# Kernel tuning notes

Hardware: AMD Instinct MI355X
Metric: run time of the kernel (lower is better)

Reference implementation:

```python
import jax, jax.numpy as jnp
import numpy as np

EPS = 1e-6

def gram_schmidt_orthonormalize(U, eps=EPS):
    # U: [B, K, D] -> orthonormalized along K, vectorized over batch
    B, K, D = U.shape
    vs = []
    for i in range(K):
        v = U[:, i]  # [B, D]
        for vj in vs:
            coeff = jnp.sum(v * vj, axis=1, keepdims=True) / (jnp.sum(vj * vj, axis=1, keepdims=True) + eps)
            v = v - coeff * vj
        norm = jnp.maximum(jnp.linalg.norm(v, axis=1, keepdims=True), eps)
        vs.append(v / norm)
    return jnp.stack(vs, axis=1)  # [B, K, D]

def setup_inputs() -> dict:
    key = jax.random.key(0)
    ks = jax.random.split(key, 14)
    B, IN, H1, H2, OUT, E, G = 4096, 1024, 2048, 2048, 512, 8, 256
    s = 0.02
    return {
        "x":   jax.random.normal(ks[0], (B, IN), jnp.float32),
        "W1":  jax.random.normal(ks[1], (E, IN, H1), jnp.float32) * s,
        "b1":  jnp.zeros((E, H1), jnp.float32),
        "W2":  jax.random.normal(ks[2], (E, H1, H2), jnp.float32) * s,
        "b2":  jnp.zeros((E, H2), jnp.float32),
        "W3":  jax.random.normal(ks[3], (E, H2, OUT), jnp.float32) * s,
        "b3":  jnp.zeros((E, OUT), jnp.float32),
        "Wg1": jax.random.normal(ks[4], (IN, G), jnp.float32) * s,
        "bg1": jnp.zeros((G,), jnp.float32),
        "Wg2": jax.random.normal(ks[5], (G, E), jnp.float32) * s,
        "bg2": jnp.zeros((E,), jnp.float32),
        "Wo":  jax.random.normal(ks[6], (OUT, 1), jnp.float32) * s,
        "bo":  jnp.zeros((1,), jnp.float32),
    }

def reference(x, W1, b1, W2, b2, W3, b3, Wg1, bg1, Wg2, bg2, Wo, bo):
    # Expert MLPs, batched over expert axis e: [B,E,h]
    h = jax.nn.relu(jnp.einsum('bi,eih->beh', x, W1) + b1)
    h = jax.nn.relu(jnp.einsum('beh,ehk->bek', h, W2) + b2)
    expert_outputs = jnp.einsum('bek,ekd->bed', h, W3) + b3  # [B, E, D]
    # Gating network: MLP + softmax over experts
    g = jax.nn.relu(x @ Wg1 + bg1)
    gate_weights = jax.nn.softmax(g @ Wg2 + bg2, axis=-1)  # [B, E]
    # Per-sample Gram-Schmidt across experts, weighted combine
    ortho = gram_schmidt_orthonormalize(expert_outputs)  # [B, E, D]
    combined = jnp.einsum('bed,be->bd', ortho, gate_weights)  # [B, D]
    final = combined @ Wo + bo  # [B, 1]
    return (final, 0.0)
```

## Files before the change

### kernel.cpp

```cpp
#include <hip/hip_runtime.h>
#include <hip/hip_bf16.h>

#define DEVINL __device__ __forceinline__

constexpr int Bsz = 4096, INF = 1024, H1 = 2048, H2 = 2048, OUTD = 512, NE = 8, G = 256;

typedef __attribute__((ext_vector_type(8))) short bf16x8;
typedef __attribute__((ext_vector_type(4))) float f32x4;
typedef __attribute__((ext_vector_type(16))) float f32x16;
typedef unsigned short u16;

DEVINL u16 f2bf(float f) {
  unsigned int u = __float_as_uint(f);
  u = (u + 0x7FFFu + ((u >> 16) & 1u)) >> 16;
  return (u16)u;
}
DEVINL float bf2f(u16 h) { return __uint_as_float((unsigned int)h << 16); }

DEVINL void gload16(const void* g, void* l) {
  __builtin_amdgcn_global_load_lds(
      (const __attribute__((address_space(1))) void*)g,
      (__attribute__((address_space(3))) void*)l, 16, 0, 0);
}

DEVINL float waveAllSum(float v) {
#pragma unroll
  for (int m = 32; m > 0; m >>= 1) v += __shfl_xor(v, m, 64);
  return v;
}

DEVINL f32x16 mfma3(bf16x8 bh, bf16x8 bl, bf16x8 ah, bf16x8 al, f32x16 c) {
  c = __builtin_amdgcn_mfma_f32_32x32x16_bf16(bh, ah, c, 0, 0, 0);
  c = __builtin_amdgcn_mfma_f32_32x32x16_bf16(bl, ah, c, 0, 0, 0);
  c = __builtin_amdgcn_mfma_f32_32x32x16_bf16(bh, al, c, 0, 0, 0);
  return c;
}

__global__ __launch_bounds__(256) void pack_wt(const float* __restrict__ W,
                                               u16* __restrict__ Th,
                                               u16* __restrict__ Tl,
                                               int K, int N) {
  __shared__ float t[32][33];
  const int e = blockIdx.z;
  W += (size_t)e * K * N;
  Th += (size_t)e * N * K;
  Tl += (size_t)e * N * K;
  const int n0 = blockIdx.x * 32, k0 = blockIdx.y * 32;
  const int r = threadIdx.x >> 3, c = (threadIdx.x & 7) * 4;
  float4 v = *(const float4*)&W[(size_t)(k0 + r) * N + n0 + c];
  t[r][c + 0] = v.x; t[r][c + 1] = v.y; t[r][c + 2] = v.z; t[r][c + 3] = v.w;
  __syncthreads();
  float o0 = t[c + 0][r], o1 = t[c + 1][r], o2 = t[c + 2][r], o3 = t[c + 3][r];
  short4 h, l;
  h.x = f2bf(o0); l.x = f2bf(o0 - bf2f(h.x));
  h.y = f2bf(o1); l.y = f2bf(o1 - bf2f(h.y));
  h.z = f2bf(o2); l.z = f2bf(o2 - bf2f(h.z));
  h.w = f2bf(o3); l.w = f2bf(o3 - bf2f(h.w));
  *(short4*)&Th[(size_t)(n0 + r) * K + k0 + c] = h;
  *(short4*)&Tl[(size_t)(n0 + r) * K + k0 + c] = l;
}

__global__ __launch_bounds__(512, 2) void gemm_2bar(
    const u16* __restrict__ Ahi, const u16* __restrict__ Alo,
    const u16* __restrict__ Bhi, const u16* __restrict__ Blo,
    const float* __restrict__ bias,
    u16* __restrict__ Chi, u16* __restrict__ Clo,
    int M, int N, int K, size_t strideAe) {
  const int e = blockIdx.x;
  Ahi += (size_t)e * strideAe;
  Alo += (size_t)e * strideAe;
  Bhi += (size_t)e * (size_t)N * K;
  Blo += (size_t)e * (size_t)N * K;
  bias += (size_t)e * N;
  Chi += (size_t)e * (size_t)M * N;
  Clo += (size_t)e * (size_t)M * N;

  const int bm = blockIdx.y * 256, bn = blockIdx.z * 256;
  __shared__ __align__(16) char ldsb[163840];
  const int lane = threadIdx.x & 63, wid = threadIdx.x >> 6;
  const int wm = wid >> 2, wn = wid & 3;
  const int l15 = lane & 15, l4 = lane >> 4;
  const int bhalf = wn >> 1, jn = wn & 1;

  f32x4 acc[8][4];
#pragma unroll
  for (int i = 0; i < 8; ++i)
#pragma unroll
    for (int j = 0; j < 4; ++j) acc[i][j] = (f32x4){0.f, 0.f, 0.f, 0.f};

  const int nt = K / 32;

  auto stageA = [&](const u16* src, int T, int slot, int ldsOp) {
#pragma unroll
    for (int q = 0; q < 2; ++q) {
      const int g = wid * 2 + q;
      gload16(src + (size_t)(bm + g * 16 + l15) * K + T * 32 + l4 * 8,
              ldsb + ldsOp + slot * 16384 + g * 1024);
    }
  };
  auto stageB = [&](int T, int h) {
    const int s = T & 1;
#pragma unroll
    for (int q = 0; q < 2; ++q) {
      const int g = wid * 2 + q;
      const u16* src = (g < 8) ? Bhi : Blo;
      const int f = g & 7;
      gload16(src + (size_t)(bn + h * 128 + f * 16 + l15) * K + T * 32 + l4 * 8,
              ldsb + ((g < 8) ? 98304 : 131072) + s * 16384 + h * 8192 + f * 1024);
    }
  };

  bf16x8 ah[4], al[4], bh[4], bl[4];
  auto readA = [&](int slot, int ih) {
#pragma unroll
    for (int i = 0; i < 4; ++i) {
      const int off = slot * 16384 + wm * 8192 + (ih * 4 + i) * 1024 + lane * 16;
      ah[i] = *(const bf16x8*)(ldsb + off);
      al[i] = *(const bf16x8*)(ldsb + 49152 + off);
    }
  };
  auto readBall = [&](int sB) {
#pragma unroll
    for (int j = 0; j < 4; ++j) {
      const int off = sB * 16384 + bhalf * 8192 + (jn * 4 + j) * 1024 + lane * 16;
      bh[j] = *(const bf16x8*)(ldsb + 98304 + off);
      bl[j] = *(const bf16x8*)(ldsb + 131072 + off);
    }
  };

#define QUAD48(IH)                                                             \
  _Pragma("unroll") for (int i = 0; i < 4; ++i) {                              \
    _Pragma("unroll") for (int j = 0; j < 4; ++j) {                            \
      f32x4 a = acc[(IH)*4 + i][j];                                            \
      a = __builtin_amdgcn_mfma_f32_16x16x32_bf16(bh[j], ah[i], a, 0, 0, 0);   \
      a = __builtin_amdgcn_mfma_f32_16x16x32_bf16(bl[j], ah[i], a, 0, 0, 0);   \
      a = __builtin_amdgcn_mfma_f32_16x16x32_bf16(bh[j], al[i], a, 0, 0, 0);   \
      acc[(IH)*4 + i][j] = a;                                                  \
    }                                                                          \
  }

  stageB(0, 0); stageB(0, 1);
  stageA(Ahi, 0, 0, 0); stageA(Alo, 0, 0, 49152);
  stageB(1, 0); stageB(1, 1);
  stageA(Ahi, 1, 1, 0); stageA(Alo, 1, 1, 49152);
  asm volatile("s_waitcnt vmcnt(8)" ::: "memory");
  __builtin_amdgcn_sched_barrier(0);
  __builtin_amdgcn_s_barrier();
  __builtin_amdgcn_sched_barrier(0);

  int aS = 0, aS2 = 2;
  for (int t = 0; t < nt - 2; ++t) {
    const int sB = t & 1;
    readA(aS, 0);
    readBall(sB);
    __builtin_amdgcn_sched_barrier(0);
    stageA(Ahi, t + 2, aS2, 0); stageA(Alo, t + 2, aS2, 49152);
    QUAD48(0);
    __builtin_amdgcn_sched_barrier(0);
    __builtin_amdgcn_s_barrier();
    __builtin_amdgcn_sched_barrier(0);
    readA(aS, 1);
    __builtin_amdgcn_sched_barrier(0);
    stageB(t + 2, 0); stageB(t + 2, 1);
    QUAD48(1);
    asm volatile("s_waitcnt vmcnt(8)" ::: "memory");
    __builtin_amdgcn_sched_barrier(0);
    __builtin_amdgcn_s_barrier();
    __builtin_amdgcn_sched_barrier(0);
    aS = (aS == 2) ? 0 : aS + 1;
    aS2 = (aS2 == 2) ? 0 : aS2 + 1;
  }
  {
    const int sB = (nt - 2) & 1;
    readA(aS, 0);
    readBall(sB);
    QUAD48(0);
    readA(aS, 1);
    QUAD48(1);
    asm volatile("s_waitcnt vmcnt(0)" ::: "memory");
    __builtin_amdgcn_sched_barrier(0);
    __builtin_amdgcn_s_barrier();
    __builtin_amdgcn_sched_barrier(0);
    aS = (aS == 2) ? 0 : aS + 1;
  }
  {
    const int sB = (nt - 1) & 1;
    readA(aS, 0);
    readBall(sB);
    QUAD48(0);
    readA(aS, 1);
    QUAD48(1);
  }
#undef QUAD48

#pragma unroll
  for (int i = 0; i < 8; ++i) {
    const int grow = bm + wm * 128 + i * 16 + l15;
#pragma unroll
    for (int j = 0; j < 4; ++j) {
      const int gcol = bn + wn * 64 + j * 16 + l4 * 4;
      const float4 bb = *(const float4*)&bias[gcol];
      float v0 = fmaxf(acc[i][j][0] + bb.x, 0.f);
      float v1 = fmaxf(acc[i][j][1] + bb.y, 0.f);
      float v2 = fmaxf(acc[i][j][2] + bb.z, 0.f);
      float v3 = fmaxf(acc[i][j][3] + bb.w, 0.f);
      short4 h, l;
      h.x = f2bf(v0); l.x = f2bf(v0 - bf2f(h.x));
      h.y = f2bf(v1); l.y = f2bf(v1 - bf2f(h.y));
      h.z = f2bf(v2); l.z = f2bf(v2 - bf2f(h.z));
      h.w = f2bf(v3); l.w = f2bf(v3 - bf2f(h.w));
      *(short4*)&Chi[(size_t)grow * N + gcol] = h;
      *(short4*)&Clo[(size_t)grow * N + gcol] = l;
    }
  }
}

__global__ __launch_bounds__(512, 2) void gemm32_128(
    const u16* __restrict__ Ahi, const u16* __restrict__ Alo,
    const u16* __restrict__ Bhi, const u16* __restrict__ Blo,
    const float* __restrict__ bias, float* __restrict__ Cf,
    int M, int N, int K, size_t strideAe) {
  const int e = blockIdx.x;
  Ahi += (size_t)e * strideAe;
  Alo += (size_t)e * strideAe;
  Bhi += (size_t)e * (size_t)N * K;
  Blo += (size_t)e * (size_t)N * K;
  bias += (size_t)e * N;
  Cf += (size_t)e * (size_t)M * N;

  const int bm = blockIdx.y * 128, bn = blockIdx.z * 256;
  __shared__ __align__(16) char ldsb[131072];
  const int lane = threadIdx.x & 63, wid = threadIdx.x >> 6;
  const int wm = wid >> 2, wn = wid & 3;
  const int l31 = lane & 31, lk = lane >> 5;

  f32x16 acc[2][2];
#pragma unroll
  for (int i = 0; i < 2; ++i)
#pragma unroll
    for (int j = 0; j < 2; ++j)
#pragma unroll
      for (int q = 0; q < 16; ++q) acc[i][j][q] = 0.f;

  const int nt = K / 32;

  auto stageA2 = [&](int T) {
    const int s = T & 1;
#pragma unroll
    for (int q = 0; q < 2; ++q) {
      const int g = wid * 2 + q;
      const u16* src = (g < 8) ? Ahi : Alo;
      const int f = g & 7;
      gload16(src + (size_t)(bm + (f >> 1) * 32 + l31) * K + T * 32 + (f & 1) * 16 + lk * 8,
              ldsb + ((g < 8) ? 0 : 16384) + s * 8192 + f * 1024);
    }
  };
  auto stageB2 = [&](int T, int slot) {
#pragma unroll
    for (int q = 0; q < 4; ++q) {
      const int g = wid * 4 + q;
      const u16* src = (g < 16) ? Bhi : Blo;
      const int f = g & 15;
      gload16(src + (size_t)(bn + (f >> 1) * 32 + l31) * K + T * 32 + (f & 1) * 16 + lk * 8,
              ldsb + ((g < 16) ? 32768 : 81920) + slot * 16384 + f * 1024);
    }
  };

  bf16x8 ah[2][2], al[2][2], b0h[2], b0l[2], b1h[2], b1l[2];
  auto readA2 = [&](int s) {
#pragma unroll
    for (int i = 0; i < 2; ++i)
#pragma unroll
      for (int ks = 0; ks < 2; ++ks) {
        const int off = s * 8192 + ((wm * 2 + i) * 2 + ks) * 1024 + lane * 16;
        ah[i][ks] = *(const bf16x8*)(ldsb + off);
        al[i][ks] = *(const bf16x8*)(ldsb + 16384 + off);
      }
  };
  auto readB2 = [&](int bs, int jh, bf16x8* bh, bf16x8* bl) {
#pragma unroll
    for (int ks = 0; ks < 2; ++ks) {
      const int off = bs * 16384 + ((wn * 2 + jh) * 2 + ks) * 1024 + lane * 16;
      bh[ks] = *(const bf16x8*)(ldsb + 32768 + off);
      bl[ks] = *(const bf16x8*)(ldsb + 81920 + off);
    }
  };

#define QUAD2(JH, BH, BL)                                                   \
  _Pragma("unroll") for (int i = 0; i < 2; ++i) {                           \
    _Pragma("unroll") for (int ks = 0; ks < 2; ++ks) {                      \
      acc[i][JH] = mfma3(BH[ks], BL[ks], ah[i][ks], al[i][ks], acc[i][JH]); \
    }                                                                       \
  }

  stageA2(0);
  stageB2(0, 0);
  stageB2(1, 1);
  asm volatile("s_waitcnt vmcnt(4)" ::: "memory");
  __builtin_amdgcn_sched_barrier(0);
  __builtin_amdgcn_s_barrier();
  __builtin_amdgcn_sched_barrier(0);

  int bs = 0;
  for (int t = 0; t < nt - 2; ++t) {
    const int sa = t & 1;
    int bs2 = bs - 1; if (bs2 < 0) bs2 = 2;
    readA2(sa);
    readB2(bs, 0, b0h, b0l);
    readB2(bs, 1, b1h, b1l);
    __builtin_amdgcn_sched_barrier(0);
    stageA2(t + 1);
    stageB2(t + 2, bs2);
    QUAD2(0, b0h, b0l);
    QUAD2(1, b1h, b1l);
    asm volatile("s_waitcnt vmcnt(4)" ::: "memory");
    __builtin_amdgcn_sched_barrier(0);
    __builtin_amdgcn_s_barrier();
    __builtin_amdgcn_sched_barrier(0);
    bs = (bs == 2) ? 0 : bs + 1;
  }
  {
    const int sa = (nt - 2) & 1;
    readA2(sa);
    readB2(bs, 0, b0h, b0l);
    readB2(bs, 1, b1h, b1l);
    __builtin_amdgcn_sched_barrier(0);
    stageA2(nt - 1);
    QUAD2(0, b0h, b0l);
    QUAD2(1, b1h, b1l);
    asm volatile("s_waitcnt vmcnt(0)" ::: "memory");
    __builtin_amdgcn_sched_barrier(0);
    __builtin_amdgcn_s_barrier();
    __builtin_amdgcn_sched_barrier(0);
    bs = (bs == 2) ? 0 : bs + 1;
  }
  {
    const int sa = (nt - 1) & 1;
    readA2(sa);
    readB2(bs, 0, b0h, b0l);
    readB2(bs, 1, b1h, b1l);
    QUAD2(0, b0h, b0l);
    QUAD2(1, b1h, b1l);
  }
#undef QUAD2

#pragma unroll
  for (int rt = 0; rt < 2; ++rt) {
    const int grow = bm + wm * 64 + rt * 32 + l31;
#pragma unroll
    for (int ct = 0; ct < 2; ++ct) {
      const int gcol0 = bn + wn * 64 + ct * 32;
      const f32x16 a = acc[rt][ct];
#pragma unroll
      for (int q = 0; q < 4; ++q) {
        const int c0 = gcol0 + q * 8 + lk * 4;
        const float4 bb = *(const float4*)&bias[c0];
        *(float4*)&Cf[(size_t)grow * N + c0] =
            make_float4(a[q * 4 + 0] + bb.x, a[q * 4 + 1] + bb.y,
                        a[q * 4 + 2] + bb.z, a[q * 4 + 3] + bb.w);
      }
    }
  }
}

__global__ __launch_bounds__(256) void gate1_kernel(
    const float* __restrict__ x, const float* __restrict__ Wg1,
    const float* __restrict__ bg1, float* __restrict__ g,
    u16* __restrict__ xhi, u16* __restrict__ xlo) {
  __shared__ float xs[8 * 1024];
  const int b0 = blockIdx.x * 8;
  const size_t base = (size_t)b0 * INF;
  const float* xp = x + base;
  for (int idx = threadIdx.x * 4; idx < 8 * 1024; idx += 1024) {
    float4 v = *(const float4*)&xp[idx];
    *(float4*)&xs[idx] = v;
    short4 h, l;
    h.x = f2bf(v.x); l.x = f2bf(v.x - bf2f(h.x));
    h.y = f2bf(v.y); l.y = f2bf(v.y - bf2f(h.y));
    h.z = f2bf(v.z); l.z = f2bf(v.z - bf2f(h.z));
    h.w = f2bf(v.w); l.w = f2bf(v.w - bf2f(h.w));
    *(short4*)&xhi[base + idx] = h;
    *(short4*)&xlo[base + idx] = l;
  }
  __syncthreads();
  const int t = threadIdx.x;
  float acc[8] = {0, 0, 0, 0, 0, 0, 0, 0};
  for (int i = 0; i < INF; ++i) {
    float w = Wg1[(size_t)i * G + t];
#pragma unroll
    for (int r = 0; r < 8; ++r) acc[r] = fmaf(xs[r * 1024 + i], w, acc[r]);
  }
  const float bb = bg1[t];
#pragma unroll
  for (int r = 0; r < 8; ++r)
    g[(size_t)(b0 + r) * G + t] = fmaxf(acc[r] + bb, 0.0f);
}

__global__ __launch_bounds__(64) void gate2_kernel(
    const float* __restrict__ g, const float* __restrict__ Wg2,
    const float* __restrict__ bg2, float* __restrict__ gw) {
  const int b = blockIdx.x, lane = threadIdx.x;
  float4 gv = *(const float4*)(g + (size_t)b * G + lane * 4);
  float p[8];
#pragma unroll
  for (int e = 0; e < 8; ++e) {
    int j = lane * 4;
    float s = gv.x * Wg2[(j + 0) * 8 + e] + gv.y * Wg2[(j + 1) * 8 + e] +
              gv.z * Wg2[(j + 2) * 8 + e] + gv.w * Wg2[(j + 3) * 8 + e];
    p[e] = waveAllSum(s);
  }
  if (lane == 0) {
    float l[8];
    float mx = -1e30f;
#pragma unroll
    for (int e = 0; e < 8; ++e) {
      l[e] = p[e] + bg2[e];
      mx = fmaxf(mx, l[e]);
    }
    float sum = 0.0f;
#pragma unroll
    for (int e = 0; e < 8; ++e) {
      l[e] = expf(l[e] - mx);
      sum += l[e];
    }
    float inv = 1.0f / sum;
#pragma unroll
    for (int e = 0; e < 8; ++e) gw[(size_t)b * 8 + e] = l[e] * inv;
  }
}

__global__ __launch_bounds__(256) void gs_kernel(
    const float* __restrict__ eo, const float* __restrict__ gw,
    const float* __restrict__ Wo, const float* __restrict__ bo,
    float* __restrict__ out, int CB) {
  const int lane = threadIdx.x & 63;
  const int b = blockIdx.x * 4 + (threadIdx.x >> 6);
  const size_t ES = (size_t)CB * OUTD;
  const float* base = eo + (size_t)b * OUTD + lane * 8;
  float vs[8][8];
  float denom[8];
#pragma unroll
  for (int i = 0; i < 8; ++i) {
    float cur[8];
    float4 u0 = *(const float4*)(base + (size_t)i * ES);
    float4 u1 = *(const float4*)(base + (size_t)i * ES + 4);
    cur[0] = u0.x; cur[1] = u0.y; cur[2] = u0.z; cur[3] = u0.w;
    cur[4] = u1.x; cur[5] = u1.y; cur[6] = u1.z; cur[7] = u1.w;
#pragma unroll
    for (int j = 0; j < i; ++j) {
      float dp = 0.0f;
#pragma unroll
      for (int d = 0; d < 8; ++d) dp = fmaf(cur[d], vs[j][d], dp);
      dp = waveAllSum(dp);
      float coeff = dp / (denom[j] + 1e-6f);
#pragma unroll
      for (int d = 0; d < 8; ++d) cur[d] = fmaf(-coeff, vs[j][d], cur[d]);
    }
    float nn = 0.0f;
#pragma unroll
    for (int d = 0; d < 8; ++d) nn = fmaf(cur[d], cur[d], nn);
    nn = waveAllSum(nn);
    float inv = 1.0f / fmaxf(sqrtf(nn), 1e-6f);
#pragma unroll
    for (int d = 0; d < 8; ++d) vs[i][d] = cur[d] * inv;
    float dd = 0.0f;
#pragma unroll
    for (int d = 0; d < 8; ++d) dd = fmaf(vs[i][d], vs[i][d], dd);
    denom[i] = waveAllSum(dd);
  }
  float gwv[8];
#pragma unroll
  for (int e = 0; e < 8; ++e) gwv[e] = gw[(size_t)b * 8 + e];
  float part = 0.0f;
#pragma unroll
  for (int d = 0; d < 8; ++d) {
    float c = 0.0f;
#pragma unroll
    for (int e = 0; e < 8; ++e) c = fmaf(vs[e][d], gwv[e], c);
    part = fmaf(c, Wo[lane * 8 + d], part);
  }
  part = waveAllSum(part);
  if (lane == 0) out[b] = part + bo[0];
}

extern "C" void kernel_launch(void* const* d_in, const int* in_sizes, int n_in,
                              void* d_out, int out_size, void* d_ws, size_t ws_size,
                              hipStream_t stream) {
  const float* x   = (const float*)d_in[0];
  const float* W1  = (const float*)d_in[1];
  const float* b1  = (const float*)d_in[2];
  const float* W2  = (const float*)d_in[3];
  const float* b2  = (const float*)d_in[4];
  const float* W3  = (const float*)d_in[5];
  const float* b3  = (const float*)d_in[6];
  const float* Wg1 = (const float*)d_in[7];
  const float* bg1 = (const float*)d_in[8];
  const float* Wg2 = (const float*)d_in[9];
  const float* bg2 = (const float*)d_in[10];
  const float* Wo  = (const float*)d_in[11];
  const float* bo  = (const float*)d_in[12];
  float* out = (float*)d_out;

  char* p = (char*)d_ws;
  float* gw = (float*)p;          p += (size_t)(128u << 10);
  float* g  = (float*)p;          p += (size_t)(4u << 20);
  u16* xhi = (u16*)p;             p += (size_t)Bsz * INF * 2;
  u16* xlo = (u16*)p;             p += (size_t)Bsz * INF * 2;
  u16* w1h = (u16*)p;             p += (size_t)NE * H1 * INF * 2;
  u16* w1l = (u16*)p;             p += (size_t)NE * H1 * INF * 2;
  u16* w2h = (u16*)p;             p += (size_t)NE * H2 * H1 * 2;
  u16* w2l = (u16*)p;             p += (size_t)NE * H2 * H1 * 2;
  u16* w3h = (u16*)p;             p += (size_t)NE * OUTD * H2 * 2;
  u16* w3l = (u16*)p;             p += (size_t)NE * OUTD * H2 * 2;
  const size_t fixedBytes = (size_t)(p - (char*)d_ws);

  int CB = 4096;
  while (CB > 256 && fixedBytes + (size_t)CB * (size_t)(128u << 10) > ws_size) CB >>= 1;
  u16* h1h = (u16*)p;
  u16* h1l = h1h + (size_t)NE * CB * H1;
  u16* h2h = h1l + (size_t)NE * CB * H1;
  u16* h2l = h2h + (size_t)NE * CB * H2;
  float* eo = (float*)h1h;

  hipMemsetAsync(d_out, 0, (size_t)out_size * sizeof(float), stream);

  gate1_kernel<<<Bsz / 8, 256, 0, stream>>>(x, Wg1, bg1, g, xhi, xlo);
  gate2_kernel<<<Bsz, 64, 0, stream>>>(g, Wg2, bg2, gw);

  pack_wt<<<dim3(H1 / 32, INF / 32, NE), 256, 0, stream>>>(W1, w1h, w1l, INF, H1);
  pack_wt<<<dim3(H2 / 32, H1 / 32, NE), 256, 0, stream>>>(W2, w2h, w2l, H1, H2);
  pack_wt<<<dim3(OUTD / 32, H2 / 32, NE), 256, 0, stream>>>(W3, w3h, w3l, H2, OUTD);

  for (int c0 = 0; c0 < Bsz; c0 += CB) {
    gemm_2bar<<<dim3(NE, CB / 256, H1 / 256), 512, 0, stream>>>(
        xhi + (size_t)c0 * INF, xlo + (size_t)c0 * INF, w1h, w1l, b1,
        h1h, h1l, CB, H1, INF, (size_t)0);
    gemm_2bar<<<dim3(NE, CB / 256, H2 / 256), 512, 0, stream>>>(
        h1h, h1l, w2h, w2l, b2, h2h, h2l, CB, H2, H1, (size_t)CB * H1);
    gemm32_128<<<dim3(NE, CB / 128, OUTD / 256), 512, 0, stream>>>(
        h2h, h2l, w3h, w3l, b3, eo, CB, OUTD, H2, (size_t)CB * H2);
    gs_kernel<<<CB / 4, 256, 0, stream>>>(eo, gw + (size_t)c0 * NE, Wo, bo,
                                          out + c0, CB);
  }
}
```

Measured before the change: 1.555 ms.

## Rework layer-3 GEMM to 16x16x32 MFMA with split-phase A/B pipeline

Replaces the 32x32x16 MFMA tiling in the third-layer GEMM with 16x16x32 MFMAs on a 4x4 accumulator grid per wave. The staging schedule changes from a triple-buffered B with double-buffered A to a triple-buffered A with double-buffered B, and each K-step is split into two half-phases with an extra barrier. A half of A is read per phase while all of B is held in registers. The aim is better overlap of global-to-LDS loads with MFMA work and a smaller LDS footprint, at the cost of an extra barrier per K-step. It only affects the smallest of the three GEMMs.

```diff
diff --git a/kernel.cpp b/kernel.cpp
--- a/kernel.cpp
+++ b/kernel.cpp
@@ -7,7 +7,6 @@
 
 typedef __attribute__((ext_vector_type(8))) short bf16x8;
 typedef __attribute__((ext_vector_type(4))) float f32x4;
-typedef __attribute__((ext_vector_type(16))) float f32x16;
 typedef unsigned short u16;
 
 DEVINL u16 f2bf(float f) {
@@ -27,13 +26,6 @@
 #pragma unroll
   for (int m = 32; m > 0; m >>= 1) v += __shfl_xor(v, m, 64);
   return v;
-}
-
-DEVINL f32x16 mfma3(bf16x8 bh, bf16x8 bl, bf16x8 ah, bf16x8 al, f32x16 c) {
-  c = __builtin_amdgcn_mfma_f32_32x32x16_bf16(bh, ah, c, 0, 0, 0);
-  c = __builtin_amdgcn_mfma_f32_32x32x16_bf16(bl, ah, c, 0, 0, 0);
-  c = __builtin_amdgcn_mfma_f32_32x32x16_bf16(bh, al, c, 0, 0, 0);
-  return c;
 }
 
 __global__ __launch_bounds__(256) void pack_wt(const float* __restrict__ W,
@@ -215,7 +207,7 @@
   }
 }
 
-__global__ __launch_bounds__(512, 2) void gemm32_128(
+__global__ __launch_bounds__(512, 2) void gemm_l3(
     const u16* __restrict__ Ahi, const u16* __restrict__ Alo,
     const u16* __restrict__ Bhi, const u16* __restrict__ Blo,
     const float* __restrict__ bias, float* __restrict__ Cf,
@@ -229,136 +221,135 @@
   Cf += (size_t)e * (size_t)M * N;
 
   const int bm = blockIdx.y * 128, bn = blockIdx.z * 256;
-  __shared__ __align__(16) char ldsb[131072];
+  __shared__ __align__(16) char ldsb[114688];
   const int lane = threadIdx.x & 63, wid = threadIdx.x >> 6;
   const int wm = wid >> 2, wn = wid & 3;
-  const int l31 = lane & 31, lk = lane >> 5;
-
-  f32x16 acc[2][2];
-#pragma unroll
-  for (int i = 0; i < 2; ++i)
-#pragma unroll
-    for (int j = 0; j < 2; ++j)
-#pragma unroll
-      for (int q = 0; q < 16; ++q) acc[i][j][q] = 0.f;
+  const int l15 = lane & 15, l4 = lane >> 4;
+  const int bhalf = wn >> 1, jn = wn & 1;
+
+  f32x4 acc[4][4];
+#pragma unroll
+  for (int i = 0; i < 4; ++i)
+#pragma unroll
+    for (int j = 0; j < 4; ++j) acc[i][j] = (f32x4){0.f, 0.f, 0.f, 0.f};
 
   const int nt = K / 32;
 
-  auto stageA2 = [&](int T) {
-    const int s = T & 1;
+  auto stageA3 = [&](int T, int slot) {
 #pragma unroll
     for (int q = 0; q < 2; ++q) {
       const int g = wid * 2 + q;
       const u16* src = (g < 8) ? Ahi : Alo;
       const int f = g & 7;
-      gload16(src + (size_t)(bm + (f >> 1) * 32 + l31) * K + T * 32 + (f & 1) * 16 + lk * 8,
-              ldsb + ((g < 8) ? 0 : 16384) + s * 8192 + f * 1024);
-    }
-  };
-  auto stageB2 = [&](int T, int slot) {
-#pragma unroll
-    for (int q = 0; q < 4; ++q) {
-      const int g = wid * 4 + q;
-      const u16* src = (g < 16) ? Bhi : Blo;
-      const int f = g & 15;
-      gload16(src + (size_t)(bn + (f >> 1) * 32 + l31) * K + T * 32 + (f & 1) * 16 + lk * 8,
-              ldsb + ((g < 16) ? 32768 : 81920) + slot * 16384 + f * 1024);
-    }
-  };
-
-  bf16x8 ah[2][2], al[2][2], b0h[2], b0l[2], b1h[2], b1l[2];
-  auto readA2 = [&](int s) {
-#pragma unroll
-    for (int i = 0; i < 2; ++i)
-#pragma unroll
-      for (int ks = 0; ks < 2; ++ks) {
-        const int off = s * 8192 + ((wm * 2 + i) * 2 + ks) * 1024 + lane * 16;
-        ah[i][ks] = *(const bf16x8*)(ldsb + off);
-        al[i][ks] = *(const bf16x8*)(ldsb + 16384 + off);
-      }
-  };
-  auto readB2 = [&](int bs, int jh, bf16x8* bh, bf16x8* bl) {
-#pragma unroll
-    for (int ks = 0; ks < 2; ++ks) {
-      const int off = bs * 16384 + ((wn * 2 + jh) * 2 + ks) * 1024 + lane * 16;
-      bh[ks] = *(const bf16x8*)(ldsb + 32768 + off);
-      bl[ks] = *(const bf16x8*)(ldsb + 81920 + off);
-    }
-  };
-
-#define QUAD2(JH, BH, BL)                                                   \
-  _Pragma("unroll") for (int i = 0; i < 2; ++i) {                           \
-    _Pragma("unroll") for (int ks = 0; ks < 2; ++ks) {                      \
-      acc[i][JH] = mfma3(BH[ks], BL[ks], ah[i][ks], al[i][ks], acc[i][JH]); \
-    }                                                                       \
-  }
-
-  stageA2(0);
-  stageB2(0, 0);
-  stageB2(1, 1);
-  asm volatile("s_waitcnt vmcnt(4)" ::: "memory");
+      gload16(src + (size_t)(bm + f * 16 + l15) * K + T * 32 + l4 * 8,
+              ldsb + ((g < 8) ? 0 : 24576) + slot * 8192 + f * 1024);
+    }
+  };
+  auto stageB = [&](int T, int h) {
+    const int s = T & 1;
+#pragma unroll
+    for (int q = 0; q < 2; ++q) {
+      const int g = wid * 2 + q;
+      const u16* src = (g < 8) ? Bhi : Blo;
+      const int f = g & 7;
+      gload16(src + (size_t)(bn + h * 128 + f * 16 + l15) * K + T * 32 + l4 * 8,
+              ldsb + ((g < 8) ? 49152 : 81920) + s * 16384 + h * 8192 + f * 1024);
+    }
+  };
+
+  bf16x8 ah[2], al[2], bh[4], bl[4];
+  auto readA = [&](int slot, int ih) {
+#pragma unroll
+    for (int i = 0; i < 2; ++i) {
+      const int off = slot * 8192 + (wm * 4 + ih * 2 + i) * 1024 + lane * 16;
+      ah[i] = *(const bf16x8*)(ldsb + off);
+      al[i] = *(const bf16x8*)(ldsb + 24576 + off);
+    }
+  };
+  auto readBall = [&](int sB) {
+#pragma unroll
+    for (int j = 0; j < 4; ++j) {
+      const int off = sB * 16384 + bhalf * 8192 + (jn * 4 + j) * 1024 + lane * 16;
+      bh[j] = *(const bf16x8*)(ldsb + 49152 + off);
+      bl[j] = *(const bf16x8*)(ldsb + 81920 + off);
+    }
+  };
+
+#define QUAD24(IH)                                                             \
+  _Pragma("unroll") for (int i = 0; i < 2; ++i) {                              \
+    _Pragma("unroll") for (int j = 0; j < 4; ++j) {                            \
+      f32x4 a = acc[(IH)*2 + i][j];                                            \
+      a = __builtin_amdgcn_mfma_f32_16x16x32_bf16(bh[j], ah[i], a, 0, 0, 0);   \
+      a = __builtin_amdgcn_mfma_f32_16x16x32_bf16(bl[j], ah[i], a, 0, 0, 0);   \
+      a = __builtin_amdgcn_mfma_f32_16x16x32_bf16(bh[j], al[i], a, 0, 0, 0);   \
+      acc[(IH)*2 + i][j] = a;                                                  \
+    }                                                                          \
+  }
+
+  stageB(0, 0); stageB(0, 1);
+  stageA3(0, 0);
+  stageB(1, 0); stageB(1, 1);
+  stageA3(1, 1);
+  asm volatile("s_waitcnt vmcnt(6)" ::: "memory");
   __builtin_amdgcn_sched_barrier(0);
   __builtin_amdgcn_s_barrier();
   __builtin_amdgcn_sched_barrier(0);
 
-  int bs = 0;
+  int aS = 0, aS2 = 2;
   for (int t = 0; t < nt - 2; ++t) {
-    const int sa = t & 1;
-    int bs2 = bs - 1; if (bs2 < 0) bs2 = 2;
-    readA2(sa);
-    readB2(bs, 0, b0h, b0l);
-    readB2(bs, 1, b1h, b1l);
-    __builtin_amdgcn_sched_barrier(0);
-    stageA2(t + 1);
-    stageB2(t + 2, bs2);
-    QUAD2(0, b0h, b0l);
-    QUAD2(1, b1h, b1l);
-    asm volatile("s_waitcnt vmcnt(4)" ::: "memory");
+    const int sB = t & 1;
+    readA(aS, 0);
+    readBall(sB);
+    __builtin_amdgcn_sched_barrier(0);
+    stageA3(t + 2, aS2);
+    QUAD24(0);
     __builtin_amdgcn_sched_barrier(0);
     __builtin_amdgcn_s_barrier();
     __builtin_amdgcn_sched_barrier(0);
-    bs = (bs == 2) ? 0 : bs + 1;
+    readA(aS, 1);
+    __builtin_amdgcn_sched_barrier(0);
+    stageB(t + 2, 0); stageB(t + 2, 1);
+    QUAD24(1);
+    asm volatile("s_waitcnt vmcnt(6)" ::: "memory");
+    __builtin_amdgcn_sched_barrier(0);
+    __builtin_amdgcn_s_barrier();
+    __builtin_amdgcn_sched_barrier(0);
+    aS = (aS == 2) ? 0 : aS + 1;
+    aS2 = (aS2 == 2) ? 0 : aS2 + 1;
   }
   {
-    const int sa = (nt - 2) & 1;
-    readA2(sa);
-    readB2(bs, 0, b0h, b0l);
-    readB2(bs, 1, b1h, b1l);
-    __builtin_amdgcn_sched_barrier(0);
-    stageA2(nt - 1);
-    QUAD2(0, b0h, b0l);
-    QUAD2(1, b1h, b1l);
+    const int sB = (nt - 2) & 1;
+    readA(aS, 0);
+    readBall(sB);
+    QUAD24(0);
+    readA(aS, 1);
+    QUAD24(1);
     asm volatile("s_waitcnt vmcnt(0)" ::: "memory");
     __builtin_amdgcn_sched_barrier(0);
     __builtin_amdgcn_s_barrier();
     __builtin_amdgcn_sched_barrier(0);
-    bs = (bs == 2) ? 0 : bs + 1;
+    aS = (aS == 2) ? 0 : aS + 1;
   }
   {
-    const int sa = (nt - 1) & 1;
-    readA2(sa);
-    readB2(bs, 0, b0h, b0l);
-    readB2(bs, 1, b1h, b1l);
-    QUAD2(0, b0h, b0l);
-    QUAD2(1, b1h, b1l);
-  }
-#undef QUAD2
-
-#pragma unroll
-  for (int rt = 0; rt < 2; ++rt) {
-    const int grow = bm + wm * 64 + rt * 32 + l31;
-#pragma unroll
-    for (int ct = 0; ct < 2; ++ct) {
-      const int gcol0 = bn + wn * 64 + ct * 32;
-      const f32x16 a = acc[rt][ct];
-#pragma unroll
-      for (int q = 0; q < 4; ++q) {
-        const int c0 = gcol0 + q * 8 + lk * 4;
-        const float4 bb = *(const float4*)&bias[c0];
-        *(float4*)&Cf[(size_t)grow * N + c0] =
-            make_float4(a[q * 4 + 0] + bb.x, a[q * 4 + 1] + bb.y,
-                        a[q * 4 + 2] + bb.z, a[q * 4 + 3] + bb.w);
-      }
+    const int sB = (nt - 1) & 1;
+    readA(aS, 0);
+    readBall(sB);
+    QUAD24(0);
+    readA(aS, 1);
+    QUAD24(1);
+  }
+#undef QUAD24
+
+#pragma unroll
+  for (int i = 0; i < 4; ++i) {
+    const int grow = bm + wm * 64 + i * 16 + l15;
+#pragma unroll
+    for (int j = 0; j < 4; ++j) {
+      const int gcol = bn + wn * 64 + j * 16 + l4 * 4;
+      const float4 bb = *(const float4*)&bias[gcol];
+      *(float4*)&Cf[(size_t)grow * N + gcol] =
+          make_float4(acc[i][j][0] + bb.x, acc[i][j][1] + bb.y,
+                      acc[i][j][2] + bb.z, acc[i][j][3] + bb.w);
     }
   }
 }
@@ -537,7 +528,7 @@
         h1h, h1l, CB, H1, INF, (size_t)0);
     gemm_2bar<<<dim3(NE, CB / 256, H2 / 256), 512, 0, stream>>>(
         h1h, h1l, w2h, w2l, b2, h2h, h2l, CB, H2, H1, (size_t)CB * H1);
-    gemm32_128<<<dim3(NE, CB / 128, OUTD / 256), 512, 0, stream>>>(
+    gemm_l3<<<dim3(NE, CB / 128, OUTD / 256), 512, 0, stream>>>(
         h2h, h2l, w3h, w3l, b3, eo, CB, OUTD, H2, (size_t)CB * H2);
     gs_kernel<<<CB / 4, 256, 0, stream>>>(eo, gw + (size_t)c0 * NE, Wo, bo,
                                           out + c0, CB);
```

After: 1.523 ms, median of 2. -2.1%, faster.
